# Performance work log

Hardware: AMD Instinct MI355X
Metric: run time of the kernel (lower is better)

Reference implementation:

```python
import jax, jax.numpy as jnp
import numpy as np
from jax import lax

# static config
P = 16          # patch_len
S = 8           # stride_base
MAX_OFF = 4.0


def setup_inputs() -> dict:
    key = jax.random.key(0)
    ks = jax.random.split(key, 7)
    B, L, N, A, D = 64, 512, 64, 64, 256
    x = jax.random.normal(ks[0], (B, L, N), dtype=jnp.float32)
    conv_w = jax.random.normal(ks[1], (32, N, 3), dtype=jnp.float32) * 0.05
    conv_b = jnp.zeros((32,), dtype=jnp.float32)
    lin_w = jax.random.normal(ks[2], (A, 32), dtype=jnp.float32) * 0.1
    lin_b = jnp.zeros((A,), dtype=jnp.float32)
    wp_w = jax.random.normal(ks[3], (D, P), dtype=jnp.float32) * 0.1
    wp_b = jnp.zeros((D,), dtype=jnp.float32)
    return {"x": x, "conv_w": conv_w, "conv_b": conv_b,
            "lin_w": lin_w, "lin_b": lin_b, "wp_w": wp_w, "wp_b": wp_b}


def _forward(x, conv_w, conv_b, lin_w, lin_b, wp_w, wp_b):
    B, L, N = x.shape
    A = lin_w.shape[0]
    D = wp_w.shape[0]
    z = jnp.transpose(x, (0, 2, 1))  # (B, N, L) -- channels = series

    # offset head: Conv1d(N->32, k=3, pad=1) -> ReLU -> global avg pool -> Linear(32->A)
    h = lax.conv_general_dilated(z, conv_w, window_strides=(1,),
                                 padding=[(1, 1)],
                                 dimension_numbers=("NCH", "OIH", "NCH"))
    h = jax.nn.relu(h + conv_b[None, :, None])      # (B, 32, L)
    pooled = jnp.mean(h, axis=-1)                    # (B, 32)
    delta = MAX_OFF * jnp.tanh(pooled @ lin_w.T + lin_b)  # (B, A)

    # sampling positions: anchor + offset + centered patch index, clamped to [0, L-1]
    anchors = jnp.arange(A, dtype=jnp.float32) * S
    pidx = jnp.arange(P, dtype=jnp.float32) - (P - 1) / 2.0
    xs = anchors[None, :, None] + delta[:, :, None] + pidx[None, None, :]  # (B, A, P)
    xs = jnp.clip(xs, 0.0, float(L - 1))

    # 1D bilinear gather (equivalent to grid_sample with y=0, border pad, align_corners=True)
    i0 = jnp.floor(xs).astype(jnp.int32)
    f = xs - i0.astype(xs.dtype)                     # (B, A, P)
    i1 = jnp.minimum(i0 + 1, L - 1)
    gather = jax.vmap(lambda zb, ib: zb[:, ib])      # (N,L),(A,P) -> (N,A,P)
    g0 = gather(z, i0)                               # (B, N, A, P)
    g1 = gather(z, i1)
    samp = g0 * (1.0 - f)[:, None] + g1 * f[:, None]  # (B, N, A, P)

    # patch projection W_P: (P -> D)
    out = jnp.einsum("bnap,dp->bnad", samp, wp_w) + wp_b  # (B, N, A, D)
    return out.reshape(B * N, A, D)


def reference(x, conv_w, conv_b, lin_w, lin_b, wp_w, wp_b):
    return _forward(x, conv_w, conv_b, lin_w, lin_b, wp_w, wp_b)
```

## Files before the change

kernel.cpp:

```cpp
#include <hip/hip_runtime.h>
#include <hip/hip_bf16.h>
#include <cmath>

#define BB 64
#define LL 512
#define NN 64
#define AA 64
#define PP 16
#define DD 256
#define MAX_OFF 4.0f
#define STRIDE_S 8

typedef __attribute__((ext_vector_type(8))) short short8_t;
typedef __attribute__((ext_vector_type(4))) float float4_t;

static __device__ __forceinline__ unsigned f2bf(float x) {
    union { float f; unsigned u; } v; v.f = x;
    return (v.u + 0x7FFFu + ((v.u >> 16) & 1u)) >> 16;
}

__global__ __launch_bounds__(256) void conv_pool_kernel(
    const float* __restrict__ x,
    const float* __restrict__ conv_w,
    const float* __restrict__ conv_b,
    float* __restrict__ pool_partial)
{
    const int c = blockIdx.x;
    const int b = blockIdx.y;
    const int t = threadIdx.x;

    __shared__ float4 wl[3 * 16 * 32];
    __shared__ float  xl[66 * 64];
    __shared__ float  red[8][32];

    for (int idx = t; idx < 1536; idx += 256) {
        int o  = idx & 31;
        int nv = (idx >> 5) & 15;
        int k  = idx >> 9;
        float4 v;
        v.x = conv_w[(o * 64 + nv * 4 + 0) * 3 + k];
        v.y = conv_w[(o * 64 + nv * 4 + 1) * 3 + k];
        v.z = conv_w[(o * 64 + nv * 4 + 2) * 3 + k];
        v.w = conv_w[(o * 64 + nv * 4 + 3) * 3 + k];
        wl[idx] = v;
    }

    const int base_row = c * 64 - 1;
    for (int idx = t; idx < 66 * 16; idx += 256) {
        int j  = idx >> 4;
        int nv = idx & 15;
        int row = base_row + j;
        float4 v = make_float4(0.f, 0.f, 0.f, 0.f);
        if (row >= 0 && row < LL)
            v = *reinterpret_cast<const float4*>(&x[((size_t)b * LL + row) * NN + nv * 4]);
        *reinterpret_cast<float4*>(&xl[j * 64 + nv * 4]) = v;
    }
    __syncthreads();

    const int o  = t & 31;
    const int lg = t >> 5;

    float s[8];
#pragma unroll
    for (int j = 0; j < 8; ++j) s[j] = 0.f;

#pragma unroll
    for (int nv = 0; nv < 16; ++nv) {
        float4 xv[10];
#pragma unroll
        for (int j = 0; j < 10; ++j)
            xv[j] = *reinterpret_cast<const float4*>(&xl[(lg * 8 + j) * 64 + nv * 4]);
#pragma unroll
        for (int k = 0; k < 3; ++k) {
            float4 w4 = wl[(k * 16 + nv) * 32 + o];
#pragma unroll
            for (int j = 0; j < 8; ++j) {
                s[j] = fmaf(xv[j + k].x, w4.x, s[j]);
                s[j] = fmaf(xv[j + k].y, w4.y, s[j]);
                s[j] = fmaf(xv[j + k].z, w4.z, s[j]);
                s[j] = fmaf(xv[j + k].w, w4.w, s[j]);
            }
        }
    }

    const float cb = conv_b[o];
    float part = 0.f;
#pragma unroll
    for (int j = 0; j < 8; ++j) part += fmaxf(s[j] + cb, 0.f);
    red[lg][o] = part;
    __syncthreads();

    if (t < 32) {
        float sum = 0.f;
#pragma unroll
        for (int g = 0; g < 8; ++g) sum += red[g][t];
        pool_partial[((size_t)b * 8 + c) * 32 + t] = sum;
    }
}

__global__ __launch_bounds__(64) void delta_kernel(
    const float* __restrict__ pool_partial,
    const float* __restrict__ lin_w,
    const float* __restrict__ lin_b,
    const float* __restrict__ wp_w,
    float* __restrict__ delta,
    unsigned short* __restrict__ wp16)
{
    const int b = blockIdx.x;
    const int t = threadIdx.x;
    __shared__ float pooled[32];

    if (t < 32) {
        float s = 0.f;
#pragma unroll
        for (int c = 0; c < 8; ++c) s += pool_partial[((size_t)b * 8 + c) * 32 + t];
        pooled[t] = s * (1.0f / 512.0f);
    }
    __syncthreads();

    float s = lin_b[t];
#pragma unroll
    for (int o = 0; o < 32; ++o) s = fmaf(pooled[o], lin_w[t * 32 + o], s);
    delta[b * AA + t] = MAX_OFF * tanhf(s);

    if (b == 0) {
        const float4* w4 = reinterpret_cast<const float4*>(wp_w);
        uint2* o2 = reinterpret_cast<uint2*>(wp16);
#pragma unroll
        for (int i = 0; i < 16; ++i) {
            float4 v = w4[i * 64 + t];
            uint2 pk;
            pk.x = f2bf(v.x) | (f2bf(v.y) << 16);
            pk.y = f2bf(v.z) | (f2bf(v.w) << 16);
            o2[i * 64 + t] = pk;
        }
    }
}

#define XR_STRIDE 68
#define SA_ST     24

__global__ __launch_bounds__(256) void patch_proj_kernel(
    const float* __restrict__ x,
    const unsigned short* __restrict__ wp16,
    const float* __restrict__ wp_b,
    const float* __restrict__ delta,
    float* __restrict__ out)
{
    const int a = blockIdx.x;
    const int b = blockIdx.y;
    const int t = threadIdx.x;
    const int lane = t & 63;
    const int w  = t >> 6;
    const int lg = lane >> 4;
    const int lr = lane & 15;

    __shared__ float          xr[17 * XR_STRIDE];
    __shared__ unsigned short sampA[64 * SA_ST];

    const float dlt  = delta[b * AA + a];
    const float base = (float)(a * STRIDE_S) - 7.5f + dlt;
    const int   r0   = (int)floorf(base);

    for (int idx = t; idx < 17 * 16; idx += 256) {
        int j  = idx >> 4;
        int nv = idx & 15;
        int row = max(0, min(LL - 1, r0 + j));
        float4 v = *reinterpret_cast<const float4*>(&x[((size_t)b * LL + row) * NN + nv * 4]);
        *reinterpret_cast<float4*>(&xr[j * XR_STRIDE + nv * 4]) = v;
    }

    short8_t afrag[4];
    float4_t acc[4][4];
    const short8_t zero8 = {0, 0, 0, 0, 0, 0, 0, 0};
#pragma unroll
    for (int i = 0; i < 4; ++i) {
        const int d = w * 64 + i * 16 + lr;
        short8_t v = *reinterpret_cast<const short8_t*>(&wp16[d * 16 + (lg & 1) * 8]);
        afrag[i] = (lg < 2) ? v : zero8;
        float4 bv = *reinterpret_cast<const float4*>(&wp_b[w * 64 + i * 16 + lg * 4]);
        float4_t c4 = {bv.x, bv.y, bv.z, bv.w};
#pragma unroll
        for (int s = 0; s < 4; ++s) acc[s][i] = c4;
    }
    __syncthreads();

    {
        const int pp  = t & 7;
        const int nr0 = t >> 3;
        float f_[2]; int j0_[2], j1_[2];
#pragma unroll
        for (int q = 0; q < 2; ++q) {
            int p = pp * 2 + q;
            float xs = base + (float)p;
            xs = fminf(fmaxf(xs, 0.f), (float)(LL - 1));
            int i0 = (int)floorf(xs);
            f_[q]  = xs - (float)i0;
            j0_[q] = i0 - r0;
            j1_[q] = min(i0 + 1, LL - 1) - r0;
        }
#pragma unroll
        for (int h = 0; h < 2; ++h) {
            int n = nr0 + 32 * h;
            unsigned pk = 0;
#pragma unroll
            for (int q = 0; q < 2; ++q) {
                float g0 = xr[j0_[q] * XR_STRIDE + n];
                float g1 = xr[j1_[q] * XR_STRIDE + n];
                float s  = g0 + f_[q] * (g1 - g0);
                pk |= f2bf(s) << (16 * q);
            }
            *reinterpret_cast<unsigned*>(&sampA[n * SA_ST + pp * 2]) = pk;
        }
    }
    __syncthreads();

    short8_t bfrag[4];
#pragma unroll
    for (int s = 0; s < 4; ++s)
        bfrag[s] = *reinterpret_cast<const short8_t*>(
            &sampA[(s * 16 + lr) * SA_ST + (lg & 1) * 8]);

#pragma unroll
    for (int s = 0; s < 4; ++s)
#pragma unroll
        for (int i = 0; i < 4; ++i)
            acc[s][i] = __builtin_amdgcn_mfma_f32_16x16x32_bf16(
                afrag[i], bfrag[s], acc[s][i], 0, 0, 0);

    const size_t ob = (((size_t)b * NN) * AA + a) * DD + w * 64 + lg * 4;
#pragma unroll
    for (int s = 0; s < 4; ++s) {
        const int n = s * 16 + lr;
        const size_t rb = ob + (size_t)n * (AA * DD);
#pragma unroll
        for (int i = 0; i < 4; ++i)
            *reinterpret_cast<float4_t*>(&out[rb + i * 16]) = acc[s][i];
    }
}

extern "C" void kernel_launch(void* const* d_in, const int* in_sizes, int n_in,
                              void* d_out, int out_size, void* d_ws, size_t ws_size,
                              hipStream_t stream)
{
    const float* x      = (const float*)d_in[0];
    const float* conv_w = (const float*)d_in[1];
    const float* conv_b = (const float*)d_in[2];
    const float* lin_w  = (const float*)d_in[3];
    const float* lin_b  = (const float*)d_in[4];
    const float* wp_w   = (const float*)d_in[5];
    const float* wp_b   = (const float*)d_in[6];
    float* out = (float*)d_out;

    float* pool_partial = (float*)d_ws;
    float* delta        = pool_partial + 16384;
    unsigned short* wp16 = (unsigned short*)(delta + 4096);

    conv_pool_kernel<<<dim3(8, BB), 256, 0, stream>>>(x, conv_w, conv_b, pool_partial);
    delta_kernel<<<BB, 64, 0, stream>>>(pool_partial, lin_w, lin_b, wp_w, delta, wp16);
    patch_proj_kernel<<<dim3(AA, BB), 256, 0, stream>>>(x, wp16, wp_b, delta, out);
}
```

Baseline: 65.52 us.

## Split sampling into separate kernel and stream contiguous output planes in projection

Adds a sampling kernel that writes bf16 interpolated patches to a workspace buffer, and a projection kernel where each block produces one contiguous (A, D) output plane per (batch, series) pair. This replaces the old layout, where each block wrote rows spread across series with a large stride. The aim is more sequential, DRAM-friendly output writes, at the cost of an extra launch and an intermediate buffer round trip. It falls back to the old kernel if the workspace is too small.

```diff
diff --git a/kernel.cpp b/kernel.cpp
--- a/kernel.cpp
+++ b/kernel.cpp
@@ -137,6 +137,95 @@
     }
 }
 
+__global__ __launch_bounds__(64) void samp_kernel(
+    const float* __restrict__ x,
+    const float* __restrict__ delta,
+    unsigned* __restrict__ samp_dw)
+{
+    const int a    = blockIdx.x;
+    const int b    = blockIdx.y;
+    const int lane = threadIdx.x;
+
+    const float dlt  = delta[b * AA + a];
+    const float base = (float)(a * STRIDE_S) - 7.5f + dlt;
+    const float* xb  = x + (size_t)b * (LL * NN);
+
+    unsigned pk[8];
+#pragma unroll
+    for (int pq = 0; pq < 8; ++pq) {
+        unsigned v = 0;
+#pragma unroll
+        for (int q = 0; q < 2; ++q) {
+            float xs = base + (float)(pq * 2 + q);
+            xs = fminf(fmaxf(xs, 0.f), (float)(LL - 1));
+            int   i0 = (int)floorf(xs);
+            float f  = xs - (float)i0;
+            int   i1 = min(i0 + 1, LL - 1);
+            float g0 = xb[i0 * NN + lane];
+            float g1 = xb[i1 * NN + lane];
+            v |= f2bf(g0 + f * (g1 - g0)) << (16 * q);
+        }
+        pk[pq] = v;
+    }
+    unsigned* dst = samp_dw + ((size_t)(b * NN + lane) * AA + a) * 8;
+    *reinterpret_cast<uint4*>(dst + 0) = make_uint4(pk[0], pk[1], pk[2], pk[3]);
+    *reinterpret_cast<uint4*>(dst + 4) = make_uint4(pk[4], pk[5], pk[6], pk[7]);
+}
+
+__global__ __launch_bounds__(256) void stream_proj_kernel(
+    const unsigned short* __restrict__ wp16,
+    const float* __restrict__ wp_b,
+    const unsigned* __restrict__ samp_dw,
+    float* __restrict__ out)
+{
+    const int plane = blockIdx.x;
+    const int t = threadIdx.x;
+    const int lane = t & 63;
+    const int w  = t >> 6;
+    const int lg = lane >> 4;
+    const int lr = lane & 15;
+
+    short8_t afrag[4];
+    float4_t acc[4][4];
+    const short8_t zero8 = {0, 0, 0, 0, 0, 0, 0, 0};
+#pragma unroll
+    for (int i = 0; i < 4; ++i) {
+        const int d = w * 64 + i * 16 + lr;
+        short8_t v = *reinterpret_cast<const short8_t*>(&wp16[d * 16 + (lg & 1) * 8]);
+        afrag[i] = (lg < 2) ? v : zero8;
+        float4 bv = *reinterpret_cast<const float4*>(&wp_b[w * 64 + i * 16 + lg * 4]);
+        float4_t c4 = {bv.x, bv.y, bv.z, bv.w};
+#pragma unroll
+        for (int s = 0; s < 4; ++s) acc[s][i] = c4;
+    }
+
+    const unsigned* sp = samp_dw + (size_t)plane * (AA * 8);
+    short8_t bfrag[4];
+#pragma unroll
+    for (int s = 0; s < 4; ++s) {
+        const unsigned* rp = sp + (s * 16 + lr) * 8 + (lg & 1) * 4;
+        uint4 u4 = *reinterpret_cast<const uint4*>(rp);
+        union { uint4 u; short8_t s8; } uu; uu.u = u4;
+        bfrag[s] = uu.s8;
+    }
+
+#pragma unroll
+    for (int s = 0; s < 4; ++s)
+#pragma unroll
+        for (int i = 0; i < 4; ++i)
+            acc[s][i] = __builtin_amdgcn_mfma_f32_16x16x32_bf16(
+                afrag[i], bfrag[s], acc[s][i], 0, 0, 0);
+
+    const size_t ob = (size_t)plane * (AA * DD) + w * 64 + lg * 4;
+#pragma unroll
+    for (int s = 0; s < 4; ++s) {
+        const size_t rb = ob + (size_t)(s * 16 + lr) * DD;
+#pragma unroll
+        for (int i = 0; i < 4; ++i)
+            *reinterpret_cast<float4_t*>(&out[rb + i * 16]) = acc[s][i];
+    }
+}
+
 #define XR_STRIDE 68
 #define SA_ST     24
 
@@ -252,11 +341,20 @@
     const float* wp_b   = (const float*)d_in[6];
     float* out = (float*)d_out;
 
-    float* pool_partial = (float*)d_ws;
-    float* delta        = pool_partial + 16384;
-    unsigned short* wp16 = (unsigned short*)(delta + 4096);
+    char* wsb = (char*)d_ws;
+    float* pool_partial = (float*)wsb;
+    float* delta        = (float*)(wsb + 65536);
+    unsigned short* wp16 = (unsigned short*)(wsb + 81920);
+    unsigned* samp_dw   = (unsigned*)(wsb + 90112);
+    const size_t need = 90112 + (size_t)BB * NN * AA * 8 * 4;
 
     conv_pool_kernel<<<dim3(8, BB), 256, 0, stream>>>(x, conv_w, conv_b, pool_partial);
     delta_kernel<<<BB, 64, 0, stream>>>(pool_partial, lin_w, lin_b, wp_w, delta, wp16);
-    patch_proj_kernel<<<dim3(AA, BB), 256, 0, stream>>>(x, wp16, wp_b, delta, out);
-}
+
+    if (ws_size >= need) {
+        samp_kernel<<<dim3(AA, BB), 64, 0, stream>>>(x, delta, samp_dw);
+        stream_proj_kernel<<<BB * NN, 256, 0, stream>>>(wp16, wp_b, samp_dw, out);
+    } else {
+        patch_proj_kernel<<<dim3(AA, BB), 256, 0, stream>>>(x, wp16, wp_b, delta, out);
+    }
+}
```

After: 73.39 us. 12.0% more time.
